# Performance work log

Measured on AMD Instinct MI355X. Metric: run time of the kernel, lower is better.

Reference implementation:

```python
import jax, jax.numpy as jnp
import numpy as np

TOKENS = 4096
D_MODEL = 512
VOCAB = 128000
TILE = 256  # next_power_of_2_or_max(TOKENS // tile_factor=16, TOKENS) = 256


def setup_inputs() -> dict:
    key = jax.random.key(0)
    k1, k2, k3 = jax.random.split(key, 3)
    x = jax.random.normal(k1, (TOKENS, D_MODEL), dtype=jnp.float32)
    proj_weight = jax.random.normal(k2, (VOCAB, D_MODEL), dtype=jnp.float32) * 0.02
    target = jax.random.randint(k3, (TOKENS,), 0, VOCAB)
    return {"x": x, "proj_weight": proj_weight, "target": target}


def _tiled_max_sumexp(x, w, tile):
    # Tiled over tokens (lax.map is sequential under jit -> never materializes
    # the full [tokens, vocab] logits, matching the fused-CE memory behavior).
    n_tiles = x.shape[0] // tile
    xt = x.reshape(n_tiles, tile, x.shape[1])

    def chunk(xi):
        logits = jnp.matmul(xi, w.T).astype(jnp.float32)  # [tile, vocab]
        m = logits.max(axis=1)                            # fp_max path
        s = jnp.exp(logits - m[:, None]).sum(axis=1)      # fp_sum path
        return m, s

    m, s = jax.lax.map(chunk, xt)
    return m.reshape(-1), s.reshape(-1)  # [tokens], [tokens]


def reference(x, proj_weight, target):
    # maxs / exp-sums over vocab (online-softmax statistics)
    maxs, sums = _tiled_max_sumexp(x, proj_weight, TILE)
    # target score: gather target rows of W, dot with input (fp_target=True)
    tw = proj_weight[target]                                # [tokens, d_model]
    target_score = (x * tw).astype(jnp.float32).sum(axis=1)  # [tokens]
    # prob = softmax numerator over denominator; log_softmax=True, reduction='sum'
    prob = jnp.exp(target_score - maxs) / sums
    loss = -jnp.log(prob).sum()
    return loss
```

## Files before the change

### kernel.cpp

```cpp
#include <hip/hip_runtime.h>
#include <hip/hip_bf16.h>
#include <stdint.h>

#define TOKENS 4096
#define DM     512
#define VOCAB  128000
#define BN     128
#define BM     512
#define NCHUNK (VOCAB / BN)
#define NTILE  (TOKENS / BM)

#define XBF_OFF  0
#define PART_OFF (TOKENS * DM * 2)
#define T_OFF    (PART_OFF + NCHUNK * TOKENS * 4)
#define LDS_BYTES (BN * DM * 2)

typedef __attribute__((ext_vector_type(8))) short short8;
typedef __attribute__((ext_vector_type(4))) float f32x4;

__device__ __forceinline__ unsigned short f2bf(float f) {
  unsigned u;
  __builtin_memcpy(&u, &f, 4);
  u += 0x7fffu + ((u >> 16) & 1u);
  return (unsigned short)(u >> 16);
}

__global__ void cvt_x_kernel(const float* __restrict__ x,
                             unsigned short* __restrict__ xb,
                             float* __restrict__ out) {
  int i = (blockIdx.x * 256 + threadIdx.x) * 4;
  float4 v = *(const float4*)(x + i);
  ushort4 o;
  o.x = f2bf(v.x); o.y = f2bf(v.y); o.z = f2bf(v.z); o.w = f2bf(v.w);
  *(ushort4*)(xb + i) = o;
  if (blockIdx.x == 0 && threadIdx.x == 0) out[0] = 0.0f;
}

__global__ __launch_bounds__(512, 2) void gemm_sumexp_kernel(
    const float* __restrict__ W, const unsigned short* __restrict__ Xb,
    float* __restrict__ part) {
  extern __shared__ char smem[];
  short8* Wl = (short8*)smem;

  const int tid  = threadIdx.x;
  const int c    = blockIdx.x;
  const int lane = tid & 63;
  const int w    = tid >> 6;
  const int ln   = lane & 15;
  const int quad = lane >> 4;

  {
    const float* Wg = W + (size_t)c * BN * DM;
    #pragma unroll
    for (int it = 0; it < 16; ++it) {
      int b  = it * 512 + tid;
      int n  = b >> 6;
      int kb = b & 63;
      const f32x4* p = (const f32x4*)(Wg + n * DM + kb * 8);
      f32x4 v0 = __builtin_nontemporal_load(p);
      f32x4 v1 = __builtin_nontemporal_load(p + 1);
      short8 s;
      s[0] = (short)f2bf(v0[0]); s[1] = (short)f2bf(v0[1]);
      s[2] = (short)f2bf(v0[2]); s[3] = (short)f2bf(v0[3]);
      s[4] = (short)f2bf(v1[0]); s[5] = (short)f2bf(v1[1]);
      s[6] = (short)f2bf(v1[2]); s[7] = (short)f2bf(v1[3]);
      int S = kb >> 2, q = kb & 3;
      Wl[(n >> 4) * 1024 + S * 64 + q * 16 + ((n & 15) ^ (S & 7))] = s;
    }
  }
  __syncthreads();

  #pragma unroll 1
  for (int t = 0; t < NTILE; ++t) {
    f32x4 acc[8][4];
    #pragma unroll
    for (int i = 0; i < 8; ++i)
      #pragma unroll
      for (int j = 0; j < 4; ++j)
        acc[i][j] = f32x4{0.f, 0.f, 0.f, 0.f};

    const unsigned short* xrow =
        Xb + (size_t)(t * BM + w * 64 + ln) * DM + quad * 8;

    short8 bfA[4], bfB[4];
    #pragma unroll
    for (int j = 0; j < 4; ++j)
      bfA[j] = *(const short8*)(xrow + j * 16 * DM);

    #pragma unroll 1
    for (int sp = 0; sp < 8; ++sp) {
      const int s0 = 2 * sp, s1 = 2 * sp + 1;
      #pragma unroll
      for (int j = 0; j < 4; ++j)
        bfB[j] = *(const short8*)(xrow + j * 16 * DM + s1 * 32);
      {
        short8 af[8];
        const int rb = s0 * 64 + (lane ^ (s0 & 7));
        #pragma unroll
        for (int i = 0; i < 8; ++i) af[i] = Wl[i * 1024 + rb];
        __builtin_amdgcn_s_setprio(1);
        #pragma unroll
        for (int i = 0; i < 8; ++i)
          #pragma unroll
          for (int j = 0; j < 4; ++j)
            acc[i][j] = __builtin_amdgcn_mfma_f32_16x16x32_bf16(
                af[i], bfA[j], acc[i][j], 0, 0, 0);
        __builtin_amdgcn_s_setprio(0);
      }
      #pragma unroll
      for (int j = 0; j < 4; ++j)
        bfA[j] = *(const short8*)(xrow + j * 16 * DM + (s0 + 2) * 32);
      {
        short8 af[8];
        const int rb = s1 * 64 + (lane ^ (s1 & 7));
        #pragma unroll
        for (int i = 0; i < 8; ++i) af[i] = Wl[i * 1024 + rb];
        __builtin_amdgcn_s_setprio(1);
        #pragma unroll
        for (int i = 0; i < 8; ++i)
          #pragma unroll
          for (int j = 0; j < 4; ++j)
            acc[i][j] = __builtin_amdgcn_mfma_f32_16x16x32_bf16(
                af[i], bfB[j], acc[i][j], 0, 0, 0);
        __builtin_amdgcn_s_setprio(0);
      }
    }

    #pragma unroll
    for (int j = 0; j < 4; ++j) {
      float e = 0.f;
      #pragma unroll
      for (int i = 0; i < 8; ++i) {
        #pragma unroll
        for (int r = 0; r < 4; ++r) e += __expf(acc[i][j][r]);
      }
      e += __shfl_xor(e, 16, 64);
      e += __shfl_xor(e, 32, 64);
      if (lane < 16) {
        float* pp = part + (size_t)c * TOKENS + t * BM + w * 64 + j * 16 + lane;
        __builtin_nontemporal_store(e, pp);
      }
    }
  }
}

__global__ void target_dot_kernel(const float* __restrict__ x,
                                  const float* __restrict__ W,
                                  const int* __restrict__ tgt,
                                  float* __restrict__ T) {
  int wave = threadIdx.x >> 6, lane = threadIdx.x & 63;
  int i = blockIdx.x * 4 + wave;
  int r = tgt[i];
  const float4* xp = (const float4*)(x + (size_t)i * DM + lane * 8);
  const float4* wp = (const float4*)(W + (size_t)r * DM + lane * 8);
  float4 a0 = xp[0], a1 = xp[1], b0 = wp[0], b1 = wp[1];
  float s = a0.x * b0.x + a0.y * b0.y + a0.z * b0.z + a0.w * b0.w
          + a1.x * b1.x + a1.y * b1.y + a1.z * b1.z + a1.w * b1.w;
  #pragma unroll
  for (int m = 32; m >= 1; m >>= 1) s += __shfl_xor(s, m, 64);
  if (lane == 0) T[i] = s;
}

__global__ void reduce_loss_kernel(const float* __restrict__ part,
                                   const float* __restrict__ T,
                                   float* __restrict__ out) {
  __shared__ float red[256];
  int tid = threadIdx.x;
  int tok = blockIdx.x * 64 + (tid & 63);
  int g = tid >> 6;
  float S = 0.f;
  #pragma unroll 5
  for (int cc = g; cc < NCHUNK; cc += 4) S += part[cc * TOKENS + tok];
  red[tid] = S;
  __syncthreads();
  if (tid < 64) {
    float Sa = red[tid] + red[64 + tid] + red[128 + tid] + red[192 + tid];
    float loss = __logf(Sa) - T[tok];
    #pragma unroll
    for (int m = 32; m >= 1; m >>= 1) loss += __shfl_xor(loss, m, 64);
    if (tid == 0) atomicAdd(out, loss);
  }
}

extern "C" void kernel_launch(void* const* d_in, const int* in_sizes, int n_in,
                              void* d_out, int out_size, void* d_ws, size_t ws_size,
                              hipStream_t stream) {
  const float* x   = (const float*)d_in[0];
  const float* W   = (const float*)d_in[1];
  const int*   tgt = (const int*)d_in[2];
  float* out = (float*)d_out;

  unsigned short* xb   = (unsigned short*)((char*)d_ws + XBF_OFF);
  float*          part = (float*)((char*)d_ws + PART_OFF);
  float*          T    = (float*)((char*)d_ws + T_OFF);

  hipFuncSetAttribute(reinterpret_cast<const void*>(gemm_sumexp_kernel),
                      hipFuncAttributeMaxDynamicSharedMemorySize, LDS_BYTES);

  cvt_x_kernel<<<TOKENS * DM / (256 * 4), 256, 0, stream>>>(x, xb, out);
  gemm_sumexp_kernel<<<NCHUNK, 512, LDS_BYTES, stream>>>(W, xb, part);
  target_dot_kernel<<<TOKENS / 4, 256, 0, stream>>>(x, W, tgt, T);
  reduce_loss_kernel<<<TOKENS / 64, 256, 0, stream>>>(part, T, out);
}
```

Before: 863.9 us.

## Split GEMM-sumexp block into 16 waves across vocab halves with LDS partial combine

The workgroup grows from 8 to 16 waves. Each pair of waves covers the same 64 tokens, with each wave taking half of the 128 vocab rows in the chunk, so the per-wave accumulator tile drops from 8x4 to 4x4. The two partial exp-sums are combined through a small LDS scratch area, guarded by two barriers, before the store to global. The manual double-buffering of the X fragments is dropped in favour of a simple per-step load. This is meant to add latency hiding and lower register pressure, at the cost of extra barriers, reloading X twice as often, and less load/compute overlap.

```diff
diff --git a/kernel.cpp b/kernel.cpp
--- a/kernel.cpp
+++ b/kernel.cpp
@@ -6,14 +6,14 @@
 #define DM     512
 #define VOCAB  128000
 #define BN     128
-#define BM     512
+#define BMT    512
 #define NCHUNK (VOCAB / BN)
-#define NTILE  (TOKENS / BM)
+#define NTILE  (TOKENS / BMT)
 
 #define XBF_OFF  0
 #define PART_OFF (TOKENS * DM * 2)
 #define T_OFF    (PART_OFF + NCHUNK * TOKENS * 4)
-#define LDS_BYTES (BN * DM * 2)
+#define LDS_BYTES (BN * DM * 2 + BMT * 2 * 4)
 
 typedef __attribute__((ext_vector_type(8))) short short8;
 typedef __attribute__((ext_vector_type(4))) float f32x4;
@@ -36,24 +36,27 @@
   if (blockIdx.x == 0 && threadIdx.x == 0) out[0] = 0.0f;
 }
 
-__global__ __launch_bounds__(512, 2) void gemm_sumexp_kernel(
+__global__ __launch_bounds__(1024, 4) void gemm_sumexp_kernel(
     const float* __restrict__ W, const unsigned short* __restrict__ Xb,
     float* __restrict__ part) {
   extern __shared__ char smem[];
   short8* Wl = (short8*)smem;
+  float*  sc = (float*)(smem + BN * DM * 2);
 
   const int tid  = threadIdx.x;
   const int c    = blockIdx.x;
   const int lane = tid & 63;
   const int w    = tid >> 6;
+  const int tg   = w & 7;
+  const int rg   = w >> 3;
   const int ln   = lane & 15;
   const int quad = lane >> 4;
 
   {
     const float* Wg = W + (size_t)c * BN * DM;
     #pragma unroll
-    for (int it = 0; it < 16; ++it) {
-      int b  = it * 512 + tid;
+    for (int it = 0; it < 8; ++it) {
+      int b  = it * 1024 + tid;
       int n  = b >> 6;
       int kb = b & 63;
       const f32x4* p = (const f32x4*)(Wg + n * DM + kb * 8);
@@ -72,74 +75,58 @@
 
   #pragma unroll 1
   for (int t = 0; t < NTILE; ++t) {
-    f32x4 acc[8][4];
+    f32x4 acc[4][4];
     #pragma unroll
-    for (int i = 0; i < 8; ++i)
+    for (int i = 0; i < 4; ++i)
       #pragma unroll
       for (int j = 0; j < 4; ++j)
         acc[i][j] = f32x4{0.f, 0.f, 0.f, 0.f};
 
     const unsigned short* xrow =
-        Xb + (size_t)(t * BM + w * 64 + ln) * DM + quad * 8;
-
-    short8 bfA[4], bfB[4];
-    #pragma unroll
-    for (int j = 0; j < 4; ++j)
-      bfA[j] = *(const short8*)(xrow + j * 16 * DM);
+        Xb + (size_t)(t * BMT + tg * 64 + ln) * DM + quad * 8;
 
     #pragma unroll 1
-    for (int sp = 0; sp < 8; ++sp) {
-      const int s0 = 2 * sp, s1 = 2 * sp + 1;
+    for (int s = 0; s < DM / 32; ++s) {
+      short8 bf[4], af[4];
       #pragma unroll
       for (int j = 0; j < 4; ++j)
-        bfB[j] = *(const short8*)(xrow + j * 16 * DM + s1 * 32);
-      {
-        short8 af[8];
-        const int rb = s0 * 64 + (lane ^ (s0 & 7));
+        bf[j] = *(const short8*)(xrow + j * 16 * DM + s * 32);
+      const int rb = s * 64 + (lane ^ (s & 7));
+      #pragma unroll
+      for (int i = 0; i < 4; ++i)
+        af[i] = Wl[(rg * 4 + i) * 1024 + rb];
+      __builtin_amdgcn_s_setprio(1);
+      #pragma unroll
+      for (int i = 0; i < 4; ++i)
         #pragma unroll
-        for (int i = 0; i < 8; ++i) af[i] = Wl[i * 1024 + rb];
-        __builtin_amdgcn_s_setprio(1);
-        #pragma unroll
-        for (int i = 0; i < 8; ++i)
-          #pragma unroll
-          for (int j = 0; j < 4; ++j)
-            acc[i][j] = __builtin_amdgcn_mfma_f32_16x16x32_bf16(
-                af[i], bfA[j], acc[i][j], 0, 0, 0);
-        __builtin_amdgcn_s_setprio(0);
-      }
-      #pragma unroll
-      for (int j = 0; j < 4; ++j)
-        bfA[j] = *(const short8*)(xrow + j * 16 * DM + (s0 + 2) * 32);
-      {
-        short8 af[8];
-        const int rb = s1 * 64 + (lane ^ (s1 & 7));
-        #pragma unroll
-        for (int i = 0; i < 8; ++i) af[i] = Wl[i * 1024 + rb];
-        __builtin_amdgcn_s_setprio(1);
-        #pragma unroll
-        for (int i = 0; i < 8; ++i)
-          #pragma unroll
-          for (int j = 0; j < 4; ++j)
-            acc[i][j] = __builtin_amdgcn_mfma_f32_16x16x32_bf16(
-                af[i], bfB[j], acc[i][j], 0, 0, 0);
-        __builtin_amdgcn_s_setprio(0);
-      }
+        for (int j = 0; j < 4; ++j)
+          acc[i][j] = __builtin_amdgcn_mfma_f32_16x16x32_bf16(
+              af[i], bf[j], acc[i][j], 0, 0, 0);
+      __builtin_amdgcn_s_setprio(0);
     }
 
+    float ev[4];
     #pragma unroll
     for (int j = 0; j < 4; ++j) {
       float e = 0.f;
       #pragma unroll
-      for (int i = 0; i < 8; ++i) {
+      for (int i = 0; i < 4; ++i) {
         #pragma unroll
         for (int r = 0; r < 4; ++r) e += __expf(acc[i][j][r]);
       }
       e += __shfl_xor(e, 16, 64);
       e += __shfl_xor(e, 32, 64);
-      if (lane < 16) {
-        float* pp = part + (size_t)c * TOKENS + t * BM + w * 64 + j * 16 + lane;
-        __builtin_nontemporal_store(e, pp);
-      }
+      ev[j] = e;
+    }
+    __syncthreads();
+    #pragma unroll
+    for (int j = 0; j < 4; ++j)
+      if (lane < 16) sc[rg * 512 + tg * 64 + j * 16 + lane] = ev[j];
+    __syncthreads();
+    if (tid < 512) {
+      float v = sc[tid] + sc[512 + tid];
+      float* pp = part + (size_t)c * TOKENS + t * BMT + tid;
+      __builtin_nontemporal_store(v, pp);
     }
   }
 }
@@ -198,7 +185,7 @@
                       hipFuncAttributeMaxDynamicSharedMemorySize, LDS_BYTES);
 
   cvt_x_kernel<<<TOKENS * DM / (256 * 4), 256, 0, stream>>>(x, xb, out);
-  gemm_sumexp_kernel<<<NCHUNK, 512, LDS_BYTES, stream>>>(W, xb, part);
+  gemm_sumexp_kernel<<<NCHUNK, 1024, LDS_BYTES, stream>>>(W, xb, part);
   target_dot_kernel<<<TOKENS / 4, 256, 0, stream>>>(x, W, tgt, T);
   reduce_loss_kernel<<<TOKENS / 64, 256, 0, stream>>>(part, T, out);
 }
```

New measurement: 1.302 ms. 1.51x slower.

## Switch GEMM to 32x32x16 bf16 MFMA with new LDS layout and prefetch

Applied to the files above, without the earlier changes.

Replaces the 16x16x32 MFMA tiling (8x4 fragments) with 32x32x16 MFMA (4x2 fragments of 16 floats). The LDS layout for W changes to match, using a rotation-based swizzle in place of the XOR swizzle. Both W and X fragments are now double-buffered: the next k-step's operands are loaded right after each MFMA group. The aim is fewer MFMA issues and fragment loads per FLOP, and better overlap of loads with compute, at the cost of a new layout that must avoid LDS bank conflicts.

```diff
diff --git a/kernel.cpp b/kernel.cpp
--- a/kernel.cpp
+++ b/kernel.cpp
@@ -6,9 +6,9 @@
 #define DM     512
 #define VOCAB  128000
 #define BN     128
-#define BM     512
+#define BMT    512
 #define NCHUNK (VOCAB / BN)
-#define NTILE  (TOKENS / BM)
+#define NTILE  (TOKENS / BMT)
 
 #define XBF_OFF  0
 #define PART_OFF (TOKENS * DM * 2)
@@ -17,6 +17,7 @@
 
 typedef __attribute__((ext_vector_type(8))) short short8;
 typedef __attribute__((ext_vector_type(4))) float f32x4;
+typedef __attribute__((ext_vector_type(16))) float f32x16;
 
 __device__ __forceinline__ unsigned short f2bf(float f) {
   unsigned u;
@@ -42,12 +43,12 @@
   extern __shared__ char smem[];
   short8* Wl = (short8*)smem;
 
-  const int tid  = threadIdx.x;
-  const int c    = blockIdx.x;
-  const int lane = tid & 63;
-  const int w    = tid >> 6;
-  const int ln   = lane & 15;
-  const int quad = lane >> 4;
+  const int tid   = threadIdx.x;
+  const int c     = blockIdx.x;
+  const int lane  = tid & 63;
+  const int w     = tid >> 6;
+  const int tok32 = lane & 31;
+  const int half  = lane >> 5;
 
   {
     const float* Wg = W + (size_t)c * BN * DM;
@@ -64,80 +65,92 @@
       s[2] = (short)f2bf(v0[2]); s[3] = (short)f2bf(v0[3]);
       s[4] = (short)f2bf(v1[0]); s[5] = (short)f2bf(v1[1]);
       s[6] = (short)f2bf(v1[2]); s[7] = (short)f2bf(v1[3]);
-      int S = kb >> 2, q = kb & 3;
-      Wl[(n >> 4) * 1024 + S * 64 + q * 16 + ((n & 15) ^ (S & 7))] = s;
+      int sE = kb >> 1, kh = kb & 1, rf = n >> 5, r0 = n & 31;
+      int g = sE * 4 + rf;
+      int intra = kh * 32 + r0;
+      Wl[g * 64 + ((intra + g) & 63)] = s;
     }
   }
   __syncthreads();
 
   #pragma unroll 1
   for (int t = 0; t < NTILE; ++t) {
-    f32x4 acc[8][4];
-    #pragma unroll
-    for (int i = 0; i < 8; ++i)
-      #pragma unroll
-      for (int j = 0; j < 4; ++j)
-        acc[i][j] = f32x4{0.f, 0.f, 0.f, 0.f};
-
-    const unsigned short* xrow =
-        Xb + (size_t)(t * BM + w * 64 + ln) * DM + quad * 8;
-
-    short8 bfA[4], bfB[4];
-    #pragma unroll
-    for (int j = 0; j < 4; ++j)
-      bfA[j] = *(const short8*)(xrow + j * 16 * DM);
+    f32x16 acc[4][2];
+    #pragma unroll
+    for (int i = 0; i < 4; ++i)
+      #pragma unroll
+      for (int j = 0; j < 2; ++j)
+        acc[i][j] = (f32x16)(0.f);
+
+    const unsigned short* xbase =
+        Xb + (size_t)(t * BMT + w * 64 + tok32) * DM + half * 8;
+
+    short8 bfP[2], bfQ[2], afA[4], afB[4];
+
+    #pragma unroll
+    for (int cf = 0; cf < 2; ++cf) {
+      bfP[cf] = *(const short8*)(xbase + cf * 32 * DM + 0 * 16);
+      bfQ[cf] = *(const short8*)(xbase + cf * 32 * DM + 1 * 16);
+    }
+    #pragma unroll
+    for (int rf = 0; rf < 4; ++rf) {
+      int g0 = 0 * 4 + rf, g1 = 1 * 4 + rf;
+      afA[rf] = Wl[g0 * 64 + ((lane + g0) & 63)];
+      afB[rf] = Wl[g1 * 64 + ((lane + g1) & 63)];
+    }
 
     #pragma unroll 1
-    for (int sp = 0; sp < 8; ++sp) {
-      const int s0 = 2 * sp, s1 = 2 * sp + 1;
-      #pragma unroll
-      for (int j = 0; j < 4; ++j)
-        bfB[j] = *(const short8*)(xrow + j * 16 * DM + s1 * 32);
-      {
-        short8 af[8];
-        const int rb = s0 * 64 + (lane ^ (s0 & 7));
+    for (int sp = 0; sp < 16; ++sp) {
+      const int s0  = 2 * sp, s1 = 2 * sp + 1;
+      const int sn0 = (s0 + 2) & 31;
+      const int sn1 = (s1 + 2) & 31;
+
+      __builtin_amdgcn_s_setprio(1);
+      #pragma unroll
+      for (int rf = 0; rf < 4; ++rf)
         #pragma unroll
-        for (int i = 0; i < 8; ++i) af[i] = Wl[i * 1024 + rb];
-        __builtin_amdgcn_s_setprio(1);
+        for (int cf = 0; cf < 2; ++cf)
+          acc[rf][cf] = __builtin_amdgcn_mfma_f32_32x32x16_bf16(
+              afA[rf], bfP[cf], acc[rf][cf], 0, 0, 0);
+      __builtin_amdgcn_s_setprio(0);
+      #pragma unroll
+      for (int cf = 0; cf < 2; ++cf)
+        bfP[cf] = *(const short8*)(xbase + cf * 32 * DM + sn0 * 16);
+      #pragma unroll
+      for (int rf = 0; rf < 4; ++rf) {
+        int g = sn0 * 4 + rf;
+        afA[rf] = Wl[g * 64 + ((lane + g) & 63)];
+      }
+
+      __builtin_amdgcn_s_setprio(1);
+      #pragma unroll
+      for (int rf = 0; rf < 4; ++rf)
         #pragma unroll
-        for (int i = 0; i < 8; ++i)
-          #pragma unroll
-          for (int j = 0; j < 4; ++j)
-            acc[i][j] = __builtin_amdgcn_mfma_f32_16x16x32_bf16(
-                af[i], bfA[j], acc[i][j], 0, 0, 0);
-        __builtin_amdgcn_s_setprio(0);
-      }
-      #pragma unroll
-      for (int j = 0; j < 4; ++j)
-        bfA[j] = *(const short8*)(xrow + j * 16 * DM + (s0 + 2) * 32);
-      {
-        short8 af[8];
-        const int rb = s1 * 64 + (lane ^ (s1 & 7));
+        for (int cf = 0; cf < 2; ++cf)
+          acc[rf][cf] = __builtin_amdgcn_mfma_f32_32x32x16_bf16(
+              afB[rf], bfQ[cf], acc[rf][cf], 0, 0, 0);
+      __builtin_amdgcn_s_setprio(0);
+      #pragma unroll
+      for (int cf = 0; cf < 2; ++cf)
+        bfQ[cf] = *(const short8*)(xbase + cf * 32 * DM + sn1 * 16);
+      #pragma unroll
+      for (int rf = 0; rf < 4; ++rf) {
+        int g = sn1 * 4 + rf;
+        afB[rf] = Wl[g * 64 + ((lane + g) & 63)];
+      }
+    }
+
+    #pragma unroll
+    for (int cf = 0; cf < 2; ++cf) {
+      float e = 0.f;
+      #pragma unroll
+      for (int rf = 0; rf < 4; ++rf) {
         #pragma unroll
-        for (int i = 0; i < 8; ++i) af[i] = Wl[i * 1024 + rb];
-        __builtin_amdgcn_s_setprio(1);
-        #pragma unroll
-        for (int i = 0; i < 8; ++i)
-          #pragma unroll
-          for (int j = 0; j < 4; ++j)
-            acc[i][j] = __builtin_amdgcn_mfma_f32_16x16x32_bf16(
-                af[i], bfB[j], acc[i][j], 0, 0, 0);
-        __builtin_amdgcn_s_setprio(0);
-      }
-    }
-
-    #pragma unroll
-    for (int j = 0; j < 4; ++j) {
-      float e = 0.f;
-      #pragma unroll
-      for (int i = 0; i < 8; ++i) {
-        #pragma unroll
-        for (int r = 0; r < 4; ++r) e += __expf(acc[i][j][r]);
-      }
-      e += __shfl_xor(e, 16, 64);
+        for (int r = 0; r < 16; ++r) e += __expf(acc[rf][cf][r]);
+      }
       e += __shfl_xor(e, 32, 64);
-      if (lane < 16) {
-        float* pp = part + (size_t)c * TOKENS + t * BM + w * 64 + j * 16 + lane;
+      if (lane < 32) {
+        float* pp = part + (size_t)c * TOKENS + t * BMT + w * 64 + cf * 32 + lane;
         __builtin_nontemporal_store(e, pp);
       }
     }
```

Result: slower. 918.5 us (+6.3%).
